# Kernel optimization log

Measured on AMD Instinct MI355X. Metric: run time of the kernel, lower is better.

Reference implementation:

```python
import jax, jax.numpy as jnp
import numpy as np

N_VAR = 2048   # number of variable nodes
DEG = 4        # edges per variable node
N_EDGE = N_VAR * DEG  # 8192 expanded/duplicated edge messages
BATCH = 32
DENSITY = 8.0 / N_EDGE  # sparse Tanner-style edge-edge connectivity


def setup_inputs() -> dict:
    key = jax.random.key(0)
    k1, k2, k3 = jax.random.split(key, 3)
    inp = jax.random.normal(k1, (BATCH, N_EDGE), dtype=jnp.float32)
    llr = jax.random.normal(k2, (BATCH, N_VAR), dtype=jnp.float32)
    # binary sparse mask [E_out, E_in]
    mask = (jax.random.uniform(k3, (N_EDGE, N_EDGE)) < DENSITY).astype(jnp.float32)
    # llr_expander: one-hot rows mapping each edge to its variable node [E, N_VAR]
    var_idx = jnp.tile(jnp.arange(N_VAR), DEG)
    llr_expander = jax.nn.one_hot(var_idx, N_VAR, dtype=jnp.float32)
    # learned params, initialized as in the module (ones, pre-masked)
    input_weight = mask * jnp.ones((N_EDGE, N_EDGE), dtype=jnp.float32)
    llr_weight = jnp.ones((1, N_VAR), dtype=jnp.float32)
    return {"input": inp, "input_weight": input_weight, "mask": mask,
            "llr": llr, "llr_weight": llr_weight, "llr_expander": llr_expander}


def reference(input, input_weight, mask, llr, llr_weight, llr_expander):
    # x = 0.5 * ( expand(w_llr * llr) + input @ (mask * W).T )
    weighted_input = input @ (mask * input_weight).T          # [B, E]
    expanded_llr = (llr_weight * llr) @ llr_expander.T        # [B, E]
    return 0.5 * (expanded_llr + weighted_input)
```

## Files before the change

kernel.cpp:

```cpp
#include <hip/hip_runtime.h>


#define N_VAR  2048
#define N_EDGE 8192
#define BATCH  32
#define BLOCK  256
#define CAP    128

__global__ __launch_bounds__(BLOCK) void bp_vc_kernel(
    const float* __restrict__ input,
    const float* __restrict__ weight,
    const float* __restrict__ mask,
    const float* __restrict__ llr,
    const float* __restrict__ llr_w,
    float* __restrict__ out)
{
    __shared__ float acc[BATCH];
    __shared__ int   cols[CAP];
    __shared__ float mvals[CAP];
    __shared__ int   cnt;

    const int row = blockIdx.x;
    const int tid = threadIdx.x;

    if (tid < BATCH) acc[tid] = 0.0f;
    if (tid == 0) cnt = 0;
    __syncthreads();

    const uint4* __restrict__ mrow =
        (const uint4*)(mask + (size_t)row * N_EDGE);

    uint4 m[8];
    #pragma unroll
    for (int it = 0; it < 8; ++it)
        m[it] = mrow[it * BLOCK + tid];

    #pragma unroll
    for (int it = 0; it < 8; ++it) {
        const uint4 v = m[it];
        if (v.x | v.y | v.z | v.w) {
            const unsigned c[4] = { v.x, v.y, v.z, v.w };
            const int col0 = (it * BLOCK + tid) * 4;
            #pragma unroll
            for (int j = 0; j < 4; ++j) {
                if (c[j] != 0u) {
                    const int idx = atomicAdd(&cnt, 1);
                    if (idx < CAP) {
                        cols[idx]  = col0 + j;
                        mvals[idx] = __uint_as_float(c[j]);
                    }
                }
            }
        }
    }
    __syncthreads();

    const int n = min(cnt, CAP);
    const float* __restrict__ wrow = weight + (size_t)row * N_EDGE;
    for (int i = tid; i < n * BATCH; i += BLOCK) {
        const int hit = i >> 5;
        const int b   = i & (BATCH - 1);
        const int col = cols[hit];
        const float w = mvals[hit] * wrow[col];
        atomicAdd(&acc[b], w * input[(size_t)b * N_EDGE + col]);
    }
    __syncthreads();

    if (tid < BATCH) {
        const int v = row & (N_VAR - 1);
        const float llr_term = llr_w[v] * llr[(size_t)tid * N_VAR + v];
        out[(size_t)tid * N_EDGE + row] = 0.5f * (acc[tid] + llr_term);
    }
}

extern "C" void kernel_launch(void* const* d_in, const int* in_sizes, int n_in,
                              void* d_out, int out_size, void* d_ws, size_t ws_size,
                              hipStream_t stream) {
    const float* input  = (const float*)d_in[0];
    const float* weight = (const float*)d_in[1];
    const float* mask   = (const float*)d_in[2];
    const float* llr    = (const float*)d_in[3];
    const float* llr_w  = (const float*)d_in[4];
    float* out = (float*)d_out;

    bp_vc_kernel<<<N_EDGE, BLOCK, 0, stream>>>(input, weight, mask, llr, llr_w, out);
}
```

Before: 487.2 us.

## Process one mask row per wavefront with ballot-based nonzero scan

Each 64-lane wavefront now owns one output row and scans the mask with ballot and shuffle to find nonzeros, accumulating per-batch sums in registers. This removes the shared-memory atomic compaction, the shared accumulator atomics and the block barriers. The trade-off is serialized per-hit processing inside a wave, with half the lanes redundant because the batch is 32 and the wave is 64. The per-wave mask load is also split into four rounds, which gives less memory-level parallelism per wave but four rows per block.

Result: no change. 492.4 us (+1.1%).

```diff
diff --git a/kernel.cpp b/kernel.cpp
--- a/kernel.cpp
+++ b/kernel.cpp
@@ -5,7 +5,6 @@
 #define N_EDGE 8192
 #define BATCH  32
 #define BLOCK  256
-#define CAP    128
 
 __global__ __launch_bounds__(BLOCK) void bp_vc_kernel(
     const float* __restrict__ input,
@@ -15,61 +14,53 @@
     const float* __restrict__ llr_w,
     float* __restrict__ out)
 {
-    __shared__ float acc[BATCH];
-    __shared__ int   cols[CAP];
-    __shared__ float mvals[CAP];
-    __shared__ int   cnt;
+    const int wave = threadIdx.x >> 6;
+    const int lane = threadIdx.x & 63;
+    const int row  = blockIdx.x * (BLOCK / 64) + wave;
+    const int b    = lane & (BATCH - 1);
 
-    const int row = blockIdx.x;
-    const int tid = threadIdx.x;
+    const uint4* __restrict__ mrow = (const uint4*)(mask + (size_t)row * N_EDGE);
+    const float* __restrict__ wrow = weight + (size_t)row * N_EDGE;
 
-    if (tid < BATCH) acc[tid] = 0.0f;
-    if (tid == 0) cnt = 0;
-    __syncthreads();
-
-    const uint4* __restrict__ mrow =
-        (const uint4*)(mask + (size_t)row * N_EDGE);
-
-    uint4 m[8];
-    #pragma unroll
-    for (int it = 0; it < 8; ++it)
-        m[it] = mrow[it * BLOCK + tid];
+    float acc = 0.0f;
 
     #pragma unroll
-    for (int it = 0; it < 8; ++it) {
-        const uint4 v = m[it];
-        if (v.x | v.y | v.z | v.w) {
-            const unsigned c[4] = { v.x, v.y, v.z, v.w };
-            const int col0 = (it * BLOCK + tid) * 4;
-            #pragma unroll
-            for (int j = 0; j < 4; ++j) {
-                if (c[j] != 0u) {
-                    const int idx = atomicAdd(&cnt, 1);
-                    if (idx < CAP) {
-                        cols[idx]  = col0 + j;
-                        mvals[idx] = __uint_as_float(c[j]);
+    for (int round = 0; round < 4; ++round) {
+        uint4 m[8];
+        #pragma unroll
+        for (int r = 0; r < 8; ++r)
+            m[r] = mrow[(round * 8 + r) * 64 + lane];
+
+        #pragma unroll
+        for (int r = 0; r < 8; ++r) {
+            const uint4 v = m[r];
+            unsigned long long hits = __ballot((v.x | v.y | v.z | v.w) != 0u);
+            while (hits) {
+                const int src = __builtin_ctzll(hits);
+                hits &= hits - 1;
+                const unsigned hv[4] = {
+                    (unsigned)__shfl((int)v.x, src),
+                    (unsigned)__shfl((int)v.y, src),
+                    (unsigned)__shfl((int)v.z, src),
+                    (unsigned)__shfl((int)v.w, src),
+                };
+                const int col0 = ((round * 8 + r) * 64 + src) * 4;
+                #pragma unroll
+                for (int j = 0; j < 4; ++j) {
+                    if (hv[j] != 0u) {
+                        const int col = col0 + j;
+                        const float w = __uint_as_float(hv[j]) * wrow[col];
+                        acc = fmaf(w, input[(size_t)b * N_EDGE + col], acc);
                     }
                 }
             }
         }
     }
-    __syncthreads();
 
-    const int n = min(cnt, CAP);
-    const float* __restrict__ wrow = weight + (size_t)row * N_EDGE;
-    for (int i = tid; i < n * BATCH; i += BLOCK) {
-        const int hit = i >> 5;
-        const int b   = i & (BATCH - 1);
-        const int col = cols[hit];
-        const float w = mvals[hit] * wrow[col];
-        atomicAdd(&acc[b], w * input[(size_t)b * N_EDGE + col]);
-    }
-    __syncthreads();
-
-    if (tid < BATCH) {
+    if (lane < BATCH) {
         const int v = row & (N_VAR - 1);
-        const float llr_term = llr_w[v] * llr[(size_t)tid * N_VAR + v];
-        out[(size_t)tid * N_EDGE + row] = 0.5f * (acc[tid] + llr_term);
+        const float llr_term = llr_w[v] * llr[(size_t)b * N_VAR + v];
+        out[(size_t)b * N_EDGE + row] = 0.5f * (acc + llr_term);
     }
 }
 
@@ -83,5 +74,6 @@
     const float* llr_w  = (const float*)d_in[4];
     float* out = (float*)d_out;
 
-    bp_vc_kernel<<<N_EDGE, BLOCK, 0, stream>>>(input, weight, mask, llr, llr_w, out);
+    bp_vc_kernel<<<N_EDGE / (BLOCK / 64), BLOCK, 0, stream>>>(
+        input, weight, mask, llr, llr_w, out);
 }
```
